# Performance work log

Measured on AMD Instinct MI355X. Metric: run time of the kernel, lower is better.

## Reference

```python
import jax, jax.numpy as jnp
import numpy as np

B, M, A, NS, T = 256, 16, 4096, 1024, 64
DT = 0.001          # dt
DA = DT             # da == dt
REF_T = 0.004       # refractory period (s)
SYN_DELAY_BINS = 1  # floor(syn_delay / da)
N_NEUR = 500.0      # neurons per population (self.N)
A_GRID = jnp.linspace(0.0, A * DA, A + 1)[:-1]  # (A,) ages since last spike


def _get_plam(input_total, V_old, age, rp, amem, ft):
    # V_old: (B,M,K); input_total: (B,M,1); age broadcasts against (B,M,K)
    V_new = V_old + DA * (rp - V_old) * amem + DA * input_total
    V_new = jnp.where(age < REF_T, 0.0, V_new)
    lam = jnp.where(V_new == 0.0, 1e-8, jnp.exp(V_new - ft))  # firing intensity
    p = lam * DT
    Plam = jnp.where(p >= 0.01, 1.0 - jnp.exp(-p), p)
    return V_new, Plam, lam


def setup_inputs() -> dict:
    key = jax.random.key(0)
    ks = jax.random.split(key, 13)
    return {
        "x": jax.random.normal(ks[0], (B, M), jnp.float32),
        "V_t_old": jax.random.normal(ks[1], (B, M, A), jnp.float32),
        "logS_t_old": jax.random.normal(ks[2], (B, M, A), jnp.float32),
        "sampled_neuron_v": jax.random.normal(ks[3], (B, M, NS), jnp.float32),
        "sampled_neuron_lastfire": jax.random.uniform(ks[4], (B, M, NS), jnp.float32),
        "I_syn": jax.random.uniform(ks[5], (B, M, 1), jnp.float32),
        "amem": jax.random.uniform(ks[6], (M, 1), jnp.float32),
        "asyn": jax.random.uniform(ks[7], (M, 1), jnp.float32),
        "J": jax.random.normal(ks[8], (M, M), jnp.float32),
        "rp": jax.random.uniform(ks[9], (M, 1), jnp.float32),
        "ft": jax.random.uniform(ks[10], (M, 1), jnp.float32),
        "eps": jax.random.uniform(ks[11], (1,), jnp.float32),
        "Z_hist_est": jnp.clip(jax.random.uniform(ks[12], (B, M, A + T), jnp.float32), 1e-5, 1.0),
        "internal_clock": 32,
    }


def reference(x, V_t_old, logS_t_old, sampled_neuron_v, sampled_neuron_lastfire,
              I_syn, amem, asyn, J, rp, ft, eps, Z_hist_est, internal_clock):
    clk = int(internal_clock)
    # ---- synaptic current with exponential decay and delayed pop activity ----
    exp_syn = jnp.exp(-DT * asyn)  # (M,1)
    if clk > SYN_DELAY_BINS:
        Z_t_last = Z_hist_est[:, :, clk + A - SYN_DELAY_BINS - 1:clk + A - SYN_DELAY_BINS]
        I_syn = exp_syn * I_syn + (1.0 - exp_syn) * Z_t_last / DT
    # input_total: (B,M,1)
    input_total = jnp.einsum('bm,mn->bn', I_syn[:, :, 0], J)[:, :, None] + (x * eps)[:, :, None]

    # ---- population activity update ----
    Z_t = Z_hist_est[:, :, clk:clk + A][:, :, ::-1]          # (B,M,A), youngest age first
    Z_t_new = Z_hist_est[:, :, clk + A:clk + A + 1]          # (B,M,1)

    V_t_new, Plam, _ = _get_plam(input_total, V_t_old, A_GRID, rp, amem, ft)

    S_old = jnp.exp(logS_t_old)
    m_t = S_old * Z_t
    Zmacro = jnp.sum(m_t * Plam, axis=2, keepdims=True)
    mess = 1.0 - jnp.sum(m_t, axis=2, keepdims=True)
    v_t = (1.0 - S_old) * m_t
    num = jnp.sum(v_t * Plam, axis=2, keepdims=True)
    den = jnp.sum(v_t, axis=2, keepdims=True)
    lambda_t = jnp.where(den != 0.0, num / jnp.where(den == 0.0, 1.0, den), 0.0)  # nan -> 0
    Z = jnp.clip(Zmacro + lambda_t * mess, 0.0, 1.0)
    A_t = Z / DT
    var = Z / N_NEUR + 0.1 * DT / N_NEUR
    Z_nll = 0.5 * jnp.square(Z_t_new - Z) / var + 0.5 * jnp.log(var) + 0.5 * jnp.log(2.0 * 3.14)

    # ---- sampled-neuron spike likelihood ----
    snv_new, Plam_s, lam_s = _get_plam(input_total, sampled_neuron_v, sampled_neuron_lastfire, rp, amem, ft)
    ltdt = lam_s * DT
    lnPy = jnp.where(ltdt < 0.01, snv_new - ft + jnp.log(DT), jnp.log(Plam_s))
    lnP1_y = -ltdt

    return (A_t, Z, Z_nll, lnPy, lnP1_y, V_t_new, snv_new, I_syn)
```

## Files before the change

### kernel.cpp

```cpp
#include <hip/hip_runtime.h>

#define B_   256
#define M_   16
#define A_   4096
#define NS_  1024
#define T_   64
#define AT_  (A_ + T_)

static constexpr float DTc = 0.001f;
static constexpr float DAc = 0.001f;

static constexpr size_t OFF_AT    = 0;
static constexpr size_t OFF_Z     = 4096;
static constexpr size_t OFF_ZNLL  = 8192;
static constexpr size_t OFF_LNPY  = 12288;
static constexpr size_t OFF_LNP1Y = 12288 + 4194304;
static constexpr size_t OFF_VT    = 12288 + 2ull * 4194304;
static constexpr size_t OFF_SNV   = OFF_VT + 16777216ull;
static constexpr size_t OFF_ISYN  = OFF_SNV + 4194304ull;

__global__ __launch_bounds__(256) void lif_kernel(
    const float* __restrict__ x,
    const float* __restrict__ V_t_old,
    const float* __restrict__ logS_t_old,
    const float* __restrict__ snv_in,
    const float* __restrict__ snlf,
    const float* __restrict__ I_syn,
    const float* __restrict__ amem,
    const float* __restrict__ asyn,
    const float* __restrict__ J,
    const float* __restrict__ rp,
    const float* __restrict__ ft,
    const float* __restrict__ eps,
    const float* __restrict__ Z_hist,
    const int*   __restrict__ clk_ptr,
    float* __restrict__ out)
{
    const int row = blockIdx.x;
    const int b   = row >> 4;
    const int m   = row & 15;
    const int tid = threadIdx.x;

    __shared__ float sh_I[M_];
    __shared__ float sh_inT;
    __shared__ float sh_red[4][4];

    const int clk = *clk_ptr;

    if (tid < M_) {
        float es   = expf(-DTc * asyn[tid]);
        float Iold = I_syn[b * M_ + tid];
        float In   = Iold;
        if (clk > 1) {
            float zl = Z_hist[(size_t)(b * M_ + tid) * AT_ + (clk + A_ - 2)];
            In = es * Iold + (1.0f - es) * zl / DTc;
        }
        sh_I[tid] = In;
    }
    __syncthreads();
    if (tid == 0) {
        float dot = 0.0f;
#pragma unroll
        for (int mm = 0; mm < M_; ++mm) dot += sh_I[mm] * J[mm * M_ + m];
        sh_inT = dot + x[row] * eps[0];
        out[OFF_ISYN + row] = sh_I[m];
    }
    __syncthreads();

    const float a_m  = amem[m];
    const float rp_m = rp[m];
    const float ft_m = ft[m];
    const float inT  = sh_inT;

    const size_t rowA = (size_t)row * A_;
    const size_t rowZ = (size_t)row * AT_;

    float sZm = 0.0f, sM = 0.0f, sNum = 0.0f, sDen = 0.0f;

#pragma unroll
    for (int c = 0; c < 4; ++c) {
        const int a0 = c * 1024 + tid * 4;
        const float4 vo = *reinterpret_cast<const float4*>(V_t_old    + rowA + a0);
        const float4 ls = *reinterpret_cast<const float4*>(logS_t_old + rowA + a0);
        const float vov[4] = {vo.x, vo.y, vo.z, vo.w};
        const float lsv[4] = {ls.x, ls.y, ls.z, ls.w};
        const float* zp = Z_hist + rowZ + (clk + A_ - 1 - a0);
        float vres[4];
#pragma unroll
        for (int k = 0; k < 4; ++k) {
            const int a = a0 + k;
            float V = vov[k] + DAc * (rp_m - vov[k]) * a_m + DAc * inT;
            if (a < 4) V = 0.0f;
            float lam  = (V == 0.0f) ? 1e-8f : expf(V - ft_m);
            float p    = lam * DTc;
            float Plam = (p >= 0.01f) ? (1.0f - expf(-p)) : p;
            float S    = expf(lsv[k]);
            float z    = zp[-k];
            float mt   = S * z;
            sZm += mt * Plam;
            sM  += mt;
            float v = (1.0f - S) * mt;
            sNum += v * Plam;
            sDen += v;
            vres[k] = V;
        }
        *reinterpret_cast<float4*>(out + OFF_VT + rowA + a0) =
            make_float4(vres[0], vres[1], vres[2], vres[3]);
    }

    float vals[4] = {sZm, sM, sNum, sDen};
#pragma unroll
    for (int i = 0; i < 4; ++i) {
        float v = vals[i];
        for (int off = 32; off > 0; off >>= 1) v += __shfl_down(v, off, 64);
        vals[i] = v;
    }
    const int wave = tid >> 6, lane = tid & 63;
    if (lane == 0) {
#pragma unroll
        for (int i = 0; i < 4; ++i) sh_red[wave][i] = vals[i];
    }
    __syncthreads();
    if (tid == 0) {
        float Zm  = sh_red[0][0] + sh_red[1][0] + sh_red[2][0] + sh_red[3][0];
        float sMt = sh_red[0][1] + sh_red[1][1] + sh_red[2][1] + sh_red[3][1];
        float num = sh_red[0][2] + sh_red[1][2] + sh_red[2][2] + sh_red[3][2];
        float den = sh_red[0][3] + sh_red[1][3] + sh_red[2][3] + sh_red[3][3];
        float mess  = 1.0f - sMt;
        float lam_t = (den != 0.0f) ? (num / den) : 0.0f;
        float Z = Zm + lam_t * mess;
        Z = fminf(fmaxf(Z, 0.0f), 1.0f);
        float At  = Z / DTc;
        float var = Z / 500.0f + 0.1f * DTc / 500.0f;
        float ztn = Z_hist[rowZ + clk + A_];
        float d   = ztn - Z;
        float znll = 0.5f * (d * d) / var + 0.5f * logf(var) + 0.5f * logf(2.0f * 3.14f);
        out[OFF_AT   + row] = At;
        out[OFF_Z    + row] = Z;
        out[OFF_ZNLL + row] = znll;
    }

    {
        const size_t rowS = (size_t)row * NS_;
        const int s0 = tid * 4;
        const float4 v4  = *reinterpret_cast<const float4*>(snv_in + rowS + s0);
        const float4 lf4 = *reinterpret_cast<const float4*>(snlf   + rowS + s0);
        const float vv[4] = {v4.x, v4.y, v4.z, v4.w};
        const float lf[4] = {lf4.x, lf4.y, lf4.z, lf4.w};
        float vn[4], py[4], p1[4];
#pragma unroll
        for (int k = 0; k < 4; ++k) {
            float V = vv[k] + DAc * (rp_m - vv[k]) * a_m + DAc * inT;
            if (lf[k] < 0.004f) V = 0.0f;
            float lam  = (V == 0.0f) ? 1e-8f : expf(V - ft_m);
            float ltdt = lam * DTc;
            float Plam = (ltdt >= 0.01f) ? (1.0f - expf(-ltdt)) : ltdt;
            py[k] = (ltdt < 0.01f) ? (V - ft_m + logf(DTc)) : logf(Plam);
            p1[k] = -ltdt;
            vn[k] = V;
        }
        *reinterpret_cast<float4*>(out + OFF_SNV   + rowS + s0) = make_float4(vn[0], vn[1], vn[2], vn[3]);
        *reinterpret_cast<float4*>(out + OFF_LNPY  + rowS + s0) = make_float4(py[0], py[1], py[2], py[3]);
        *reinterpret_cast<float4*>(out + OFF_LNP1Y + rowS + s0) = make_float4(p1[0], p1[1], p1[2], p1[3]);
    }
}

extern "C" void kernel_launch(void* const* d_in, const int* in_sizes, int n_in,
                              void* d_out, int out_size, void* d_ws, size_t ws_size,
                              hipStream_t stream) {
    lif_kernel<<<B_ * M_, 256, 0, stream>>>(
        (const float*)d_in[0],
        (const float*)d_in[1],
        (const float*)d_in[2],
        (const float*)d_in[3],
        (const float*)d_in[4],
        (const float*)d_in[5],
        (const float*)d_in[6],
        (const float*)d_in[7],
        (const float*)d_in[8],
        (const float*)d_in[9],
        (const float*)d_in[10],
        (const float*)d_in[11],
        (const float*)d_in[12],
        (const int*)  d_in[13],
        (float*)d_out);
}
```

Before: 309.2 us.

## Prefetch all row inputs before syncs and vectorize aligned Z_hist loads

Moves all global loads for V_t_old, logS_t_old, Z_hist and the sampled-neuron inputs to the top of the kernel, ahead of the synaptic-current setup and its barriers, so memory latency overlaps that serial prologue. When clk is a multiple of four, the reversed Z_hist window is read with float4 loads instead of scalar loads. The sampled-neuron section now runs before the block reduction. This raises register pressure because all inputs are held live across the barriers, which may lower occupancy.

```diff
diff --git a/kernel.cpp b/kernel.cpp
--- a/kernel.cpp
+++ b/kernel.cpp
@@ -47,6 +47,42 @@
 
     const int clk = *clk_ptr;
 
+    const size_t rowA = (size_t)row * A_;
+    const size_t rowZ = (size_t)row * AT_;
+    const size_t rowS = (size_t)row * NS_;
+
+    float4 vo4[4], ls4[4];
+#pragma unroll
+    for (int c = 0; c < 4; ++c) {
+        const int a0 = c * 1024 + tid * 4;
+        vo4[c] = *reinterpret_cast<const float4*>(V_t_old    + rowA + a0);
+        ls4[c] = *reinterpret_cast<const float4*>(logS_t_old + rowA + a0);
+    }
+
+    float zv[4][4];
+    const bool zAligned = ((clk & 3) == 0);
+    if (zAligned) {
+#pragma unroll
+        for (int c = 0; c < 4; ++c) {
+            const int a0 = c * 1024 + tid * 4;
+            const size_t base = rowZ + (size_t)(clk + A_ - 4 - a0);
+            const float4 w = *reinterpret_cast<const float4*>(Z_hist + base);
+            zv[c][0] = w.w; zv[c][1] = w.z; zv[c][2] = w.y; zv[c][3] = w.x;
+        }
+    } else {
+#pragma unroll
+        for (int c = 0; c < 4; ++c) {
+            const int a0 = c * 1024 + tid * 4;
+            const float* zp = Z_hist + rowZ + (clk + A_ - 1 - a0);
+#pragma unroll
+            for (int k = 0; k < 4; ++k) zv[c][k] = zp[-k];
+        }
+    }
+
+    const int s0 = tid * 4;
+    const float4 v4  = *reinterpret_cast<const float4*>(snv_in + rowS + s0);
+    const float4 lf4 = *reinterpret_cast<const float4*>(snlf   + rowS + s0);
+
     if (tid < M_) {
         float es   = expf(-DTc * asyn[tid]);
         float Iold = I_syn[b * M_ + tid];
@@ -72,19 +108,13 @@
     const float ft_m = ft[m];
     const float inT  = sh_inT;
 
-    const size_t rowA = (size_t)row * A_;
-    const size_t rowZ = (size_t)row * AT_;
-
     float sZm = 0.0f, sM = 0.0f, sNum = 0.0f, sDen = 0.0f;
 
 #pragma unroll
     for (int c = 0; c < 4; ++c) {
         const int a0 = c * 1024 + tid * 4;
-        const float4 vo = *reinterpret_cast<const float4*>(V_t_old    + rowA + a0);
-        const float4 ls = *reinterpret_cast<const float4*>(logS_t_old + rowA + a0);
-        const float vov[4] = {vo.x, vo.y, vo.z, vo.w};
-        const float lsv[4] = {ls.x, ls.y, ls.z, ls.w};
-        const float* zp = Z_hist + rowZ + (clk + A_ - 1 - a0);
+        const float vov[4] = {vo4[c].x, vo4[c].y, vo4[c].z, vo4[c].w};
+        const float lsv[4] = {ls4[c].x, ls4[c].y, ls4[c].z, ls4[c].w};
         float vres[4];
 #pragma unroll
         for (int k = 0; k < 4; ++k) {
@@ -95,8 +125,7 @@
             float p    = lam * DTc;
             float Plam = (p >= 0.01f) ? (1.0f - expf(-p)) : p;
             float S    = expf(lsv[k]);
-            float z    = zp[-k];
-            float mt   = S * z;
+            float mt   = S * zv[c][k];
             sZm += mt * Plam;
             sM  += mt;
             float v = (1.0f - S) * mt;
@@ -106,6 +135,26 @@
         }
         *reinterpret_cast<float4*>(out + OFF_VT + rowA + a0) =
             make_float4(vres[0], vres[1], vres[2], vres[3]);
+    }
+
+    {
+        const float vv[4] = {v4.x, v4.y, v4.z, v4.w};
+        const float lf[4] = {lf4.x, lf4.y, lf4.z, lf4.w};
+        float vn[4], py[4], p1[4];
+#pragma unroll
+        for (int k = 0; k < 4; ++k) {
+            float V = vv[k] + DAc * (rp_m - vv[k]) * a_m + DAc * inT;
+            if (lf[k] < 0.004f) V = 0.0f;
+            float lam  = (V == 0.0f) ? 1e-8f : expf(V - ft_m);
+            float ltdt = lam * DTc;
+            float Plam = (ltdt >= 0.01f) ? (1.0f - expf(-ltdt)) : ltdt;
+            py[k] = (ltdt < 0.01f) ? (V - ft_m + logf(DTc)) : logf(Plam);
+            p1[k] = -ltdt;
+            vn[k] = V;
+        }
+        *reinterpret_cast<float4*>(out + OFF_SNV   + rowS + s0) = make_float4(vn[0], vn[1], vn[2], vn[3]);
+        *reinterpret_cast<float4*>(out + OFF_LNPY  + rowS + s0) = make_float4(py[0], py[1], py[2], py[3]);
+        *reinterpret_cast<float4*>(out + OFF_LNP1Y + rowS + s0) = make_float4(p1[0], p1[1], p1[2], p1[3]);
     }
 
     float vals[4] = {sZm, sM, sNum, sDen};
@@ -138,30 +187,6 @@
         out[OFF_AT   + row] = At;
         out[OFF_Z    + row] = Z;
         out[OFF_ZNLL + row] = znll;
-    }
-
-    {
-        const size_t rowS = (size_t)row * NS_;
-        const int s0 = tid * 4;
-        const float4 v4  = *reinterpret_cast<const float4*>(snv_in + rowS + s0);
-        const float4 lf4 = *reinterpret_cast<const float4*>(snlf   + rowS + s0);
-        const float vv[4] = {v4.x, v4.y, v4.z, v4.w};
-        const float lf[4] = {lf4.x, lf4.y, lf4.z, lf4.w};
-        float vn[4], py[4], p1[4];
-#pragma unroll
-        for (int k = 0; k < 4; ++k) {
-            float V = vv[k] + DAc * (rp_m - vv[k]) * a_m + DAc * inT;
-            if (lf[k] < 0.004f) V = 0.0f;
-            float lam  = (V == 0.0f) ? 1e-8f : expf(V - ft_m);
-            float ltdt = lam * DTc;
-            float Plam = (ltdt >= 0.01f) ? (1.0f - expf(-ltdt)) : ltdt;
-            py[k] = (ltdt < 0.01f) ? (V - ft_m + logf(DTc)) : logf(Plam);
-            p1[k] = -ltdt;
-            vn[k] = V;
-        }
-        *reinterpret_cast<float4*>(out + OFF_SNV   + rowS + s0) = make_float4(vn[0], vn[1], vn[2], vn[3]);
-        *reinterpret_cast<float4*>(out + OFF_LNPY  + rowS + s0) = make_float4(py[0], py[1], py[2], py[3]);
-        *reinterpret_cast<float4*>(out + OFF_LNP1Y + rowS + s0) = make_float4(p1[0], p1[1], p1[2], p1[3]);
     }
 }
 
```

Result: no change. 310.0 us (+0.3%).
